# Optimization experiments

Hardware: AMD Instinct MI355X
Metric: run time of the kernel (lower is better)

Reference implementation:

```python
import jax, jax.numpy as jnp
import numpy as np

NE, NR, NT = 100000, 400, 1000000   # entities, relations, triples
B, DH, T = 32, 512, 3               # batch, hidden dim, num_steps
SELF_REL = 0                        # vocab['relation2id']['<SELF_REL>']


def setup_inputs() -> dict:
    key = jax.random.key(0)
    ks = jax.random.split(key, 10)
    questions = jax.random.randint(ks[0], (B, 1), 0, NR)
    e_s = jax.nn.one_hot(jax.random.randint(ks[1], (B,), 0, NE), NE, dtype=jnp.float32)
    answers = jax.nn.one_hot(jax.random.randint(ks[2], (B,), 0, NE), NE, dtype=jnp.float32)
    # KG triples (replaces sparse incidence matrices Msubj/Mrel/Mobj)
    subj_idx = jax.random.randint(ks[3], (NT,), 0, NE)
    rel_idx = jax.random.randint(ks[4], (NT,), 0, NR)
    obj_idx = jax.random.randint(ks[5], (NT,), 0, NE)
    # learned parameters
    rel_emb = jax.random.normal(ks[6], (NR, DH), dtype=jnp.float32) / np.float32(np.sqrt(DH))
    step_W = jax.random.normal(ks[7], (T, DH, DH), dtype=jnp.float32) * np.float32(np.sqrt(2.0 / DH))
    step_b = jnp.zeros((T, DH), dtype=jnp.float32)
    ent_emb = jax.random.normal(ks[8], (NE, DH), dtype=jnp.float32) / np.float32(np.sqrt(DH))
    ent_bias = jnp.zeros((NE,), dtype=jnp.float32)
    return dict(questions=questions, e_s=e_s, answers=answers,
                subj_idx=subj_idx, rel_idx=rel_idx, obj_idx=obj_idx,
                rel_emb=rel_emb, step_W=step_W, step_b=step_b,
                ent_emb=ent_emb, ent_bias=ent_bias)


def _follow(e, r, subj, rel, obj):
    # torch: (Mobj.T @ (Msubj @ e.T * Mrel @ r.T)).T
    x = e[:, subj] * r[:, rel]                 # [B, NT] per-triple message
    return jnp.zeros_like(e).at[:, obj].add(x)  # scatter-add to object entities


def reference(questions, e_s, answers, subj_idx, rel_idx, obj_idx,
              rel_emb, step_W, step_b, ent_emb, ent_bias):
    num_steps = step_W.shape[0]
    q_emb = rel_emb[questions[:, 0]]           # [B, DH]
    last_e = e_s
    rel_probs = []
    ent_probs = [e_s]
    for t in range(num_steps):
        cq_t = jnp.tanh(q_emb @ step_W[t].T + step_b[t])          # step encoder
        rel_dist = jax.nn.softmax(cq_t @ rel_emb.T, axis=1)       # [B, NR]
        last_e = _follow(last_e, rel_dist, subj_idx, rel_idx, obj_idx)
        if t == 0:
            gt = jnp.take_along_axis(rel_dist, questions, axis=1)  # [B,1]
            last_e = last_e - answers * gt
        rel_probs.append(rel_dist)
        # clamp scores > 1 by (detached) self-normalization
        m = (last_e > 1).astype(last_e.dtype)
        z = jax.lax.stop_gradient(m * last_e + (1 - m))
        last_e = last_e / z
        if t > 0:
            prev_rel = jnp.argmax(rel_probs[-2], axis=1)
            curr_rel = jnp.argmax(rel_probs[-1], axis=1)
            cond = (jnp.abs(prev_rel - curr_rel) == 1) & (jnp.minimum(prev_rel, curr_rel) % 2 == 0)
            m2 = cond.astype(last_e.dtype)[:, None]
            ent_m = m2 * (ent_probs[-2] > 0.9).astype(last_e.dtype)
            last_e = (1 - ent_m) * last_e
        if t == num_steps - 1:
            stack_rel = jnp.argmax(jnp.stack(rel_probs, axis=1), axis=2)  # [B, T]
            num_self = jnp.sum((stack_rel == SELF_REL).astype(jnp.int32), axis=1)
            m3 = (num_self == 1).astype(last_e.dtype)[:, None] * e_s
            last_e = (1 - m3) * last_e
        ent_probs.append(jax.lax.stop_gradient(last_e))
    e_score = last_e
    normed = e_score / (jnp.sum(e_score, axis=1, keepdims=True) + 1e-6)
    pred_e = (jax.lax.stop_gradient(normed) @ ent_emb) @ ent_emb.T + ent_bias[None, :]
    return e_score, pred_e
```

## Files before the change

### kernel.cpp

```cpp
#include <hip/hip_runtime.h>
#include <math.h>

#define NE 100000
#define NR 400
#define NT 1000000
#define B  32
#define DH 512

__global__ __launch_bounds__(256) void prep_kernel(
    const float* __restrict__ e_s, const float* __restrict__ answers,
    float* __restrict__ E0, float* __restrict__ E1,
    int* __restrict__ SRC, int* __restrict__ ANS)
{
    int bid = blockIdx.x, tid = threadIdx.x;
    __shared__ float tile[32 * 33];
    int base_e = bid * 32;
    #pragma unroll
    for (int l = 0; l < 4; ++l) {
        int idx = l * 256 + tid;
        int br = idx >> 5, ec = idx & 31;
        float v = e_s[(size_t)br * NE + base_e + ec];
        float a = answers[(size_t)br * NE + base_e + ec];
        tile[ec * 33 + br] = v;
        if (v > 0.5f) SRC[br] = base_e + ec;
        if (a > 0.5f) ANS[br] = base_e + ec;
    }
    __syncthreads();
    #pragma unroll
    for (int l = 0; l < 4; ++l) {
        int idx = l * 256 + tid;
        int ew = idx >> 5, bw = idx & 31;
        E0[(size_t)(base_e + ew) * 32 + bw] = tile[ew * 33 + bw];
        E1[(size_t)base_e * 32 + idx] = 0.f;
    }
}

__global__ __launch_bounds__(256) void stepA_kernel(
    int t,
    const int* __restrict__ questions,
    const float* __restrict__ rel_emb,
    const float* __restrict__ step_W,
    const float* __restrict__ step_b,
    float* __restrict__ RD, float* __restrict__ GT,
    int* __restrict__ AM, int* __restrict__ COND, int* __restrict__ FLAG3)
{
    __shared__ float qe[DH];
    __shared__ float cq[DH];
    __shared__ float lg[NR];
    __shared__ float rv[256];
    __shared__ int   ri[256];
    int b = blockIdx.x, tid = threadIdx.x;
    int q = questions[b];

    for (int i = tid; i < DH; i += 256) qe[i] = rel_emb[(size_t)q * DH + i];
    __syncthreads();

    for (int i = tid; i < DH; i += 256) {
        const float4* w4 = (const float4*)(step_W + ((size_t)t * DH + i) * DH);
        float acc = step_b[t * DH + i];
        for (int j = 0; j < DH / 4; ++j) {
            float4 wv = w4[j];
            acc += wv.x * qe[4*j] + wv.y * qe[4*j+1] + wv.z * qe[4*j+2] + wv.w * qe[4*j+3];
        }
        cq[i] = tanhf(acc);
    }
    __syncthreads();

    float lmax = -1e30f; int lidx = 0;
    for (int r = tid; r < NR; r += 256) {
        const float4* re4 = (const float4*)(rel_emb + (size_t)r * DH);
        float acc = 0.f;
        for (int j = 0; j < DH / 4; ++j) {
            float4 wv = re4[j];
            acc += wv.x * cq[4*j] + wv.y * cq[4*j+1] + wv.z * cq[4*j+2] + wv.w * cq[4*j+3];
        }
        lg[r] = acc;
        if (acc > lmax) { lmax = acc; lidx = r; }
    }
    rv[tid] = lmax; ri[tid] = lidx;
    __syncthreads();
    for (int s = 128; s > 0; s >>= 1) {
        if (tid < s) {
            float ov = rv[tid + s]; int oi = ri[tid + s];
            if (ov > rv[tid] || (ov == rv[tid] && oi < ri[tid])) { rv[tid] = ov; ri[tid] = oi; }
        }
        __syncthreads();
    }
    float mx = rv[0]; int amax = ri[0];
    __syncthreads();

    float lsum = 0.f;
    for (int r = tid; r < NR; r += 256) {
        float ex = expf(lg[r] - mx);
        lg[r] = ex;
        lsum += ex;
    }
    rv[tid] = lsum;
    __syncthreads();
    for (int s = 128; s > 0; s >>= 1) {
        if (tid < s) rv[tid] += rv[tid + s];
        __syncthreads();
    }
    float Z = rv[0];

    for (int r = tid; r < NR; r += 256) RD[r * B + b] = lg[r] / Z;

    if (tid == 0) {
        AM[t * B + b] = amax;
        if (t == 0) GT[b] = lg[q] / Z;
        if (t >= 1) {
            int ap = AM[(t - 1) * B + b];
            int d = ap - amax; if (d < 0) d = -d;
            int mn = ap < amax ? ap : amax;
            COND[(t - 1) * B + b] = (d == 1 && (mn % 2 == 0)) ? 1 : 0;
        }
        if (t == 2) {
            int a0 = AM[0 * B + b], a1 = AM[1 * B + b];
            int c = (a0 == 0) + (a1 == 0) + (amax == 0);
            FLAG3[b] = (c == 1) ? 1 : 0;
        }
    }
}

__global__ __launch_bounds__(256) void follow_kernel(
    const float* __restrict__ Ein, float* __restrict__ Eout,
    const float* __restrict__ RD,
    const int* __restrict__ subj, const int* __restrict__ rel,
    const int* __restrict__ obj)
{
    long long gid = (long long)blockIdx.x * 256 + threadIdx.x;
    int trip = (int)(gid >> 5);
    int b = threadIdx.x & 31;
    if (trip < NT) {
        int s = subj[trip];
        float ev = Ein[(size_t)s * 32 + b];
        if (ev != 0.f) {
            int r = rel[trip];
            int o = obj[trip];
            float x = ev * RD[r * B + b];
            if (x != 0.f) unsafeAtomicAdd(&Eout[(size_t)o * 32 + b], x);
        }
    }
}

__global__ __launch_bounds__(256) void post0_kernel(
    float* __restrict__ E1, float* __restrict__ E2,
    const int* __restrict__ ANS, const float* __restrict__ GT)
{
    int idx = blockIdx.x * 256 + threadIdx.x;
    int b = idx & 31, e = idx >> 5;
    float v = E1[idx];
    if (e == ANS[b]) v -= GT[b];
    if (v > 1.f) v = 1.f;
    E1[idx] = v;
    E2[idx] = 0.f;
}

__global__ __launch_bounds__(256) void post1_kernel(
    float* __restrict__ E2, float* __restrict__ E0,
    const int* __restrict__ COND1, const int* __restrict__ SRC,
    float* __restrict__ P, float* __restrict__ S)
{
    int idx = blockIdx.x * 256 + threadIdx.x;
    int b = idx & 31, e = idx >> 5;
    float v = E2[idx];
    if (v > 1.f) v = 1.f;
    if (COND1[b] && e == SRC[b]) v = 0.f;
    E2[idx] = v;
    E0[idx] = 0.f;
    if (idx < B * DH) P[idx] = 0.f;
    if (idx < B)      S[idx] = 0.f;
}

#define POST2_BLOCKS 512
__global__ __launch_bounds__(256) void post2_kernel(
    float* __restrict__ E0, const float* __restrict__ E1,
    const int* __restrict__ COND2, const int* __restrict__ SRC,
    const int* __restrict__ FLAG3, float* __restrict__ S)
{
    __shared__ float sS[32];
    int tid = threadIdx.x;
    int b = tid & 31;
    if (tid < 32) sS[tid] = 0.f;
    __syncthreads();

    int c2 = COND2[b];
    int f3 = FLAG3[b];
    int sr = SRC[b];

    float local = 0.f;
    for (int idx = blockIdx.x * 256 + tid; idx < NE * B; idx += POST2_BLOCKS * 256) {
        int e = idx >> 5;
        float v = E0[idx];
        if (v > 1.f) v = 1.f;
        if (c2 && E1[idx] > 0.9f) v = 0.f;
        if (f3 && e == sr) v = 0.f;
        E0[idx] = v;
        local += v;
    }
    local += __shfl_xor(local, 32, 64);
    if ((tid & 63) < 32) atomicAdd(&sS[b], local);
    __syncthreads();
    if (tid < 32) unsafeAtomicAdd(&S[tid], sS[tid]);
}

__global__ __launch_bounds__(256) void outT_kernel(
    const float* __restrict__ E0, float* __restrict__ out0)
{
    __shared__ float tile[32 * 33];
    int bid = blockIdx.x, tid = threadIdx.x;
    int base_e = bid * 32;
    #pragma unroll
    for (int l = 0; l < 4; ++l) {
        int idx = l * 256 + tid;
        int er = idx >> 5, br = idx & 31;
        tile[br * 33 + er] = E0[(size_t)(base_e + er) * 32 + br];
    }
    __syncthreads();
    #pragma unroll
    for (int l = 0; l < 4; ++l) {
        int idx = l * 256 + tid;
        int bw = idx >> 5, ew = idx & 31;
        out0[(size_t)bw * NE + base_e + ew] = tile[bw * 33 + ew];
    }
}

__global__ __launch_bounds__(256) void gemm1_kernel(
    const float* __restrict__ E0, const float* __restrict__ emb,
    float* __restrict__ P)
{
    __shared__ float evs[32 * 32];
    int tid = threadIdx.x;
    int base = blockIdx.x * 256;
    float acc0[32], acc1[32];
    #pragma unroll
    for (int b = 0; b < 32; ++b) { acc0[b] = 0.f; acc1[b] = 0.f; }
    const float2* emb2 = (const float2*)emb;

    for (int sg = 0; sg < 8; ++sg) {
        int ebase = base + sg * 32;
        __syncthreads();
        for (int k = tid; k < 1024; k += 256) {
            int ent = ebase + (k >> 5);
            evs[k] = (ent < NE) ? E0[(size_t)ent * 32 + (k & 31)] : 0.f;
        }
        __syncthreads();
        for (int i = 0; i < 32; ++i) {
            int ent = ebase + i; if (ent >= NE) ent = NE - 1;
            float2 w = emb2[(size_t)ent * 256 + tid];
            const float4* ev4 = (const float4*)(evs + i * 32);
            #pragma unroll
            for (int bg = 0; bg < 8; ++bg) {
                float4 e4 = ev4[bg];
                acc0[bg*4+0] += w.x * e4.x; acc1[bg*4+0] += w.y * e4.x;
                acc0[bg*4+1] += w.x * e4.y; acc1[bg*4+1] += w.y * e4.y;
                acc0[bg*4+2] += w.x * e4.z; acc1[bg*4+2] += w.y * e4.z;
                acc0[bg*4+3] += w.x * e4.w; acc1[bg*4+3] += w.y * e4.w;
            }
        }
    }
    int d0 = tid * 2;
    #pragma unroll
    for (int b = 0; b < 32; ++b) {
        unsafeAtomicAdd(&P[b * DH + d0],     acc0[b]);
        unsafeAtomicAdd(&P[b * DH + d0 + 1], acc1[b]);
    }
}

__global__ __launch_bounds__(256) void gemm2_kernel(
    const float* __restrict__ P, const float* __restrict__ S,
    const float* __restrict__ emb, const float* __restrict__ bias,
    float* __restrict__ out1)
{
    __shared__ float pl[B * DH];
    int tid = threadIdx.x;
    for (int k = tid; k < B * DH; k += 256) {
        int b = k >> 9;
        pl[k] = P[k] / (S[b] + 1e-6f);
    }
    __syncthreads();

    int base = blockIdx.x * 512;
    int e0 = base + tid, e1 = base + 256 + tid;
    int g0 = e0 < NE ? e0 : NE - 1;
    int g1 = e1 < NE ? e1 : NE - 1;
    const float4* emb4 = (const float4*)emb;
    const float4* pl4  = (const float4*)pl;

    float acc0[32], acc1[32];
    #pragma unroll
    for (int b = 0; b < 32; ++b) { acc0[b] = 0.f; acc1[b] = 0.f; }

    for (int dg = 0; dg < 128; ++dg) {
        float4 w0 = emb4[(size_t)g0 * 128 + dg];
        float4 w1 = emb4[(size_t)g1 * 128 + dg];
        #pragma unroll
        for (int b = 0; b < 32; ++b) {
            float4 pv = pl4[b * 128 + dg];
            acc0[b] += w0.x * pv.x + w0.y * pv.y + w0.z * pv.z + w0.w * pv.w;
            acc1[b] += w1.x * pv.x + w1.y * pv.y + w1.z * pv.z + w1.w * pv.w;
        }
    }
    float b0 = bias[g0], b1 = bias[g1];
    #pragma unroll
    for (int b = 0; b < 32; ++b) {
        if (e0 < NE) out1[(size_t)b * NE + e0] = acc0[b] + b0;
        if (e1 < NE) out1[(size_t)b * NE + e1] = acc1[b] + b1;
    }
}

extern "C" void kernel_launch(void* const* d_in, const int* in_sizes, int n_in,
                              void* d_out, int out_size, void* d_ws, size_t ws_size,
                              hipStream_t stream)
{
    const int*   questions = (const int*)d_in[0];
    const float* e_s       = (const float*)d_in[1];
    const float* answers   = (const float*)d_in[2];
    const int*   subj      = (const int*)d_in[3];
    const int*   rel       = (const int*)d_in[4];
    const int*   obj       = (const int*)d_in[5];
    const float* rel_emb   = (const float*)d_in[6];
    const float* step_W    = (const float*)d_in[7];
    const float* step_b    = (const float*)d_in[8];
    const float* ent_emb   = (const float*)d_in[9];
    const float* ent_bias  = (const float*)d_in[10];

    float* out0 = (float*)d_out;
    float* out1 = out0 + (size_t)B * NE;

    float* w  = (float*)d_ws;
    float* E0 = w;
    float* E1 = E0 + (size_t)NE * B;
    float* E2 = E1 + (size_t)NE * B;
    float* RD = E2 + (size_t)NE * B;
    float* P  = RD + NR * B;
    float* S  = P + B * DH;
    float* GT = S + B;
    int* AM    = (int*)(GT + B);
    int* COND  = AM + 3 * B;
    int* FLAG3 = COND + 2 * B;
    int* SRC   = FLAG3 + B;
    int* ANS   = SRC + B;

    const int postGrid = NE * B / 256;

    prep_kernel<<<NE / 32, 256, 0, stream>>>(e_s, answers, E0, E1, SRC, ANS);

    stepA_kernel<<<B, 256, 0, stream>>>(0, questions, rel_emb, step_W, step_b,
                                        RD, GT, AM, COND, FLAG3);
    follow_kernel<<<NT * 32 / 256, 256, 0, stream>>>(E0, E1, RD, subj, rel, obj);
    post0_kernel<<<postGrid, 256, 0, stream>>>(E1, E2, ANS, GT);

    stepA_kernel<<<B, 256, 0, stream>>>(1, questions, rel_emb, step_W, step_b,
                                        RD, GT, AM, COND, FLAG3);
    follow_kernel<<<NT * 32 / 256, 256, 0, stream>>>(E1, E2, RD, subj, rel, obj);
    post1_kernel<<<postGrid, 256, 0, stream>>>(E2, E0, COND, SRC, P, S);

    stepA_kernel<<<B, 256, 0, stream>>>(2, questions, rel_emb, step_W, step_b,
                                        RD, GT, AM, COND, FLAG3);
    follow_kernel<<<NT * 32 / 256, 256, 0, stream>>>(E2, E0, RD, subj, rel, obj);
    post2_kernel<<<POST2_BLOCKS, 256, 0, stream>>>(E0, E1, COND + B, SRC, FLAG3, S);

    outT_kernel<<<NE / 32, 256, 0, stream>>>(E0, out0);
    gemm1_kernel<<<(NE + 255) / 256, 256, 0, stream>>>(E0, ent_emb, P);
    gemm2_kernel<<<(NE + 511) / 512, 256, 0, stream>>>(P, S, ent_emb, ent_bias, out1);
}
```

Baseline: 937.9 us.

## Compact nonzero entity list in post2 and run sparse gemm1 with partial reduction

post2 now uses wave ballots to record every entity whose score row has at least one nonzero entry, collecting them into a global list through a per-block shared buffer and an atomic counter. gemm1 then walks only that list, gathering embedding rows and scores for those entities instead of streaming the whole embedding table. Each block writes its own partial sums into a scratch area reused from a free buffer, and a new reduction kernel adds them, replacing the many global atomics. This trades a small extra cost in post2, a gather pattern and an extra launch for skipping reads of embedding rows whose scores are all zero.

```diff
diff --git a/kernel.cpp b/kernel.cpp
--- a/kernel.cpp
+++ b/kernel.cpp
@@ -159,7 +159,7 @@
 __global__ __launch_bounds__(256) void post1_kernel(
     float* __restrict__ E2, float* __restrict__ E0,
     const int* __restrict__ COND1, const int* __restrict__ SRC,
-    float* __restrict__ P, float* __restrict__ S)
+    float* __restrict__ P, float* __restrict__ S, int* __restrict__ CNT)
 {
     int idx = blockIdx.x * 256 + threadIdx.x;
     int b = idx & 31, e = idx >> 5;
@@ -170,18 +170,24 @@
     E0[idx] = 0.f;
     if (idx < B * DH) P[idx] = 0.f;
     if (idx < B)      S[idx] = 0.f;
+    if (idx == 0)     CNT[0] = 0;
 }
 
 #define POST2_BLOCKS 512
 __global__ __launch_bounds__(256) void post2_kernel(
     float* __restrict__ E0, const float* __restrict__ E1,
     const int* __restrict__ COND2, const int* __restrict__ SRC,
-    const int* __restrict__ FLAG3, float* __restrict__ S)
+    const int* __restrict__ FLAG3, float* __restrict__ S,
+    int* __restrict__ LIST, int* __restrict__ CNT)
 {
     __shared__ float sS[32];
+    __shared__ int   lbuf[200];
+    __shared__ int   lcnt;
+    __shared__ int   lbase;
     int tid = threadIdx.x;
     int b = tid & 31;
     if (tid < 32) sS[tid] = 0.f;
+    if (tid == 0) lcnt = 0;
     __syncthreads();
 
     int c2 = COND2[b];
@@ -197,11 +203,22 @@
         if (f3 && e == sr) v = 0.f;
         E0[idx] = v;
         local += v;
+        unsigned long long m = __ballot(v != 0.f);
+        int lane = tid & 63;
+        if (lane == 0 && (unsigned)(m & 0xffffffffULL)) {
+            int p = atomicAdd(&lcnt, 1); lbuf[p] = e;
+        }
+        if (lane == 32 && (unsigned)(m >> 32)) {
+            int p = atomicAdd(&lcnt, 1); lbuf[p] = e;
+        }
     }
     local += __shfl_xor(local, 32, 64);
     if ((tid & 63) < 32) atomicAdd(&sS[b], local);
     __syncthreads();
     if (tid < 32) unsafeAtomicAdd(&S[tid], sS[tid]);
+    if (tid == 0) lbase = atomicAdd(CNT, lcnt);
+    __syncthreads();
+    for (int i = tid; i < lcnt; i += 256) LIST[lbase + i] = lbuf[i];
 }
 
 __global__ __launch_bounds__(256) void outT_kernel(
@@ -225,46 +242,71 @@
     }
 }
 
+#define G1_LC 128
+#define G1_BLOCKS (G1_LC * 4)
+
 __global__ __launch_bounds__(256) void gemm1_kernel(
     const float* __restrict__ E0, const float* __restrict__ emb,
-    float* __restrict__ P)
-{
-    __shared__ float evs[32 * 32];
+    const int* __restrict__ LIST, const int* __restrict__ CNT,
+    float* __restrict__ PPART)
+{
     int tid = threadIdx.x;
-    int base = blockIdx.x * 256;
-    float acc0[32], acc1[32];
-    #pragma unroll
-    for (int b = 0; b < 32; ++b) { acc0[b] = 0.f; acc1[b] = 0.f; }
+    int dc  = blockIdx.x & 3;
+    int lc  = blockIdx.x >> 2;
+    int bg  = tid >> 6;
+    int dl  = tid & 63;
+    int cnt = CNT[0];
     const float2* emb2 = (const float2*)emb;
-
-    for (int sg = 0; sg < 8; ++sg) {
-        int ebase = base + sg * 32;
-        __syncthreads();
-        for (int k = tid; k < 1024; k += 256) {
-            int ent = ebase + (k >> 5);
-            evs[k] = (ent < NE) ? E0[(size_t)ent * 32 + (k & 31)] : 0.f;
-        }
-        __syncthreads();
-        for (int i = 0; i < 32; ++i) {
-            int ent = ebase + i; if (ent >= NE) ent = NE - 1;
-            float2 w = emb2[(size_t)ent * 256 + tid];
-            const float4* ev4 = (const float4*)(evs + i * 32);
-            #pragma unroll
-            for (int bg = 0; bg < 8; ++bg) {
-                float4 e4 = ev4[bg];
-                acc0[bg*4+0] += w.x * e4.x; acc1[bg*4+0] += w.y * e4.x;
-                acc0[bg*4+1] += w.x * e4.y; acc1[bg*4+1] += w.y * e4.y;
-                acc0[bg*4+2] += w.x * e4.z; acc1[bg*4+2] += w.y * e4.z;
-                acc0[bg*4+3] += w.x * e4.w; acc1[bg*4+3] += w.y * e4.w;
-            }
-        }
-    }
-    int d0 = tid * 2;
-    #pragma unroll
-    for (int b = 0; b < 32; ++b) {
-        unsafeAtomicAdd(&P[b * DH + d0],     acc0[b]);
-        unsafeAtomicAdd(&P[b * DH + d0 + 1], acc1[b]);
-    }
+    int off2 = dc * 64 + dl;
+
+    float2 acc[8];
+    #pragma unroll
+    for (int k = 0; k < 8; ++k) { acc[k].x = 0.f; acc[k].y = 0.f; }
+
+#define G1_FMA(Wv, Ev, kk) \
+    acc[kk+0].x += Ev.x * Wv.x; acc[kk+0].y += Ev.x * Wv.y; \
+    acc[kk+1].x += Ev.y * Wv.x; acc[kk+1].y += Ev.y * Wv.y; \
+    acc[kk+2].x += Ev.z * Wv.x; acc[kk+2].y += Ev.z * Wv.y; \
+    acc[kk+3].x += Ev.w * Wv.x; acc[kk+3].y += Ev.w * Wv.y;
+
+    int i = lc;
+    for (; i + G1_LC < cnt; i += 2 * G1_LC) {
+        int ei0 = LIST[i];
+        int ei1 = LIST[i + G1_LC];
+        float2 w0 = emb2[(size_t)ei0 * 256 + off2];
+        float4 a0 = *(const float4*)(E0 + (size_t)ei0 * 32 + bg * 8);
+        float4 b0 = *(const float4*)(E0 + (size_t)ei0 * 32 + bg * 8 + 4);
+        float2 w1 = emb2[(size_t)ei1 * 256 + off2];
+        float4 a1 = *(const float4*)(E0 + (size_t)ei1 * 32 + bg * 8);
+        float4 b1 = *(const float4*)(E0 + (size_t)ei1 * 32 + bg * 8 + 4);
+        G1_FMA(w0, a0, 0) G1_FMA(w0, b0, 4)
+        G1_FMA(w1, a1, 0) G1_FMA(w1, b1, 4)
+    }
+    if (i < cnt) {
+        int ei0 = LIST[i];
+        float2 w0 = emb2[(size_t)ei0 * 256 + off2];
+        float4 a0 = *(const float4*)(E0 + (size_t)ei0 * 32 + bg * 8);
+        float4 b0 = *(const float4*)(E0 + (size_t)ei0 * 32 + bg * 8 + 4);
+        G1_FMA(w0, a0, 0) G1_FMA(w0, b0, 4)
+    }
+#undef G1_FMA
+
+    float* pp = PPART + ((size_t)lc * 32 + bg * 8) * DH + dc * 128 + dl * 2;
+    #pragma unroll
+    for (int k = 0; k < 8; ++k) *(float2*)(pp + (size_t)k * DH) = acc[k];
+}
+
+__global__ __launch_bounds__(256) void reduceP_kernel(
+    const float* __restrict__ PPART, float* __restrict__ P)
+{
+    int j = blockIdx.x * 256 + threadIdx.x;
+    const float4* pp = (const float4*)PPART;
+    float4 s; s.x = s.y = s.z = s.w = 0.f;
+    for (int lc = 0; lc < G1_LC; ++lc) {
+        float4 v = pp[(size_t)lc * (B * DH / 4) + j];
+        s.x += v.x; s.y += v.y; s.z += v.z; s.w += v.w;
+    }
+    ((float4*)P)[j] = s;
 }
 
 __global__ __launch_bounds__(256) void gemm2_kernel(
@@ -341,6 +383,9 @@
     int* FLAG3 = COND + 2 * B;
     int* SRC   = FLAG3 + B;
     int* ANS   = SRC + B;
+    int* LIST  = ANS + B;
+    int* CNT   = LIST + NE;
+    float* PPART = E2;
 
     const int postGrid = NE * B / 256;
 
@@ -354,14 +399,16 @@
     stepA_kernel<<<B, 256, 0, stream>>>(1, questions, rel_emb, step_W, step_b,
                                         RD, GT, AM, COND, FLAG3);
     follow_kernel<<<NT * 32 / 256, 256, 0, stream>>>(E1, E2, RD, subj, rel, obj);
-    post1_kernel<<<postGrid, 256, 0, stream>>>(E2, E0, COND, SRC, P, S);
+    post1_kernel<<<postGrid, 256, 0, stream>>>(E2, E0, COND, SRC, P, S, CNT);
 
     stepA_kernel<<<B, 256, 0, stream>>>(2, questions, rel_emb, step_W, step_b,
                                         RD, GT, AM, COND, FLAG3);
     follow_kernel<<<NT * 32 / 256, 256, 0, stream>>>(E2, E0, RD, subj, rel, obj);
-    post2_kernel<<<POST2_BLOCKS, 256, 0, stream>>>(E0, E1, COND + B, SRC, FLAG3, S);
+    post2_kernel<<<POST2_BLOCKS, 256, 0, stream>>>(E0, E1, COND + B, SRC, FLAG3,
+                                                   S, LIST, CNT);
 
     outT_kernel<<<NE / 32, 256, 0, stream>>>(E0, out0);
-    gemm1_kernel<<<(NE + 255) / 256, 256, 0, stream>>>(E0, ent_emb, P);
+    gemm1_kernel<<<G1_BLOCKS, 256, 0, stream>>>(E0, ent_emb, LIST, CNT, PPART);
+    reduceP_kernel<<<B * DH / 4 / 256, 256, 0, stream>>>(PPART, P);
     gemm2_kernel<<<(NE + 511) / 512, 256, 0, stream>>>(P, S, ent_emb, ent_bias, out1);
 }
```

New measurement: 863.8 us. -7.9%, faster.
